# Kernel tuning notes

Measured on AMD Instinct MI355X. Metric: run time of the kernel, lower is better.

The kernel has to match this reference:

```python
import jax, jax.numpy as jnp
import numpy as np

N, F, K, E = 50000, 128, 8, 1600000


def setup_inputs() -> dict:
    key = jax.random.key(0)
    k1, k2, k3, k4 = jax.random.split(key, 4)
    x = jax.random.normal(k1, (N, F), dtype=jnp.float32)
    adj = jax.random.randint(k2, (2, E), 0, N, dtype=jnp.int64)
    e = jax.random.normal(k3, (N, K), dtype=jnp.float32)
    stdv = 1.0 / np.sqrt(F)  # reset_parameters: uniform(-stdv, stdv)
    weights = jax.random.uniform(k4, (K, 2 * F, F), dtype=jnp.float32,
                                 minval=-stdv, maxval=stdv)
    return {"x": x, "adj": adj, "e": e, "weights": weights}


def _gcn_conv(x, row, col, n_nodes):
    # degree of each node as a message *destination* (col) -- matches torch degree(col, N)
    deg = jax.ops.segment_sum(jnp.ones(row.shape[0], x.dtype), col,
                              num_segments=n_nodes)
    val = (1.0 / jnp.sqrt(deg[col])) * (1.0 / jnp.sqrt(deg[row]))
    val = jnp.nan_to_num(val, nan=0.0, posinf=0.0, neginf=0.0)
    # SparseTensor(row=col, col=row) @ x : aggregate x[row] into col
    msg = val[:, None] * x[row]           # [E, F] gather
    return jax.ops.segment_sum(msg, col, num_segments=n_nodes)  # [N, F] scatter


def reference(x, adj, e, weights):
    n_nodes = x.shape[0]
    row, col = adj[0], adj[1]
    hi = _gcn_conv(x, row, col, n_nodes)                  # [N, F]
    hi = jnp.concatenate([hi, x], axis=1)                 # [N, 2F]
    # torch: repeat hi K times, bmm with [K,2F,F], transpose -> [N, K, F]
    outputs = jnp.einsum('nf,kfo->nko', hi, weights)      # [N, K, F]
    out = jnp.sum(e[:, :, None] * outputs, axis=1)        # gating sum over K
    out = out + x                                         # residual
    return out
```

## Files before the change

### kernel.cpp

```cpp
#include <hip/hip_runtime.h>
#include <hip/hip_bf16.h>

typedef __bf16 bf16_t;
typedef __bf16 bf16x8 __attribute__((ext_vector_type(8)));
typedef float f32x4 __attribute__((ext_vector_type(4)));
typedef float f32x2 __attribute__((ext_vector_type(2)));

#define F 128
#define KEXP 8
#define BM 256
#define BSTG 32768

#define NB 196
#define CAP 12288
#define CH 8192

__global__ __launch_bounds__(256) void k_binA(const int* __restrict__ row,
    const int* __restrict__ col, int* __restrict__ cursor,
    int* __restrict__ region, int E){
  __shared__ int stage[CH];
  __shared__ unsigned char stageb[CH];
  __shared__ int hist4[4][NB];
  __shared__ int lcur4[4][NB];
  int tid = threadIdx.x, wid = tid >> 6;
  int base = blockIdx.x * CH;
  int cnt = min(CH, E - base);
  for (int i = tid; i < 4*NB; i += 256) ((int*)hist4)[i] = 0;
  __syncthreads();
  for (int i = tid; i < cnt; i += 256){
    int r = row[base+i], c = col[base+i];
    stage[i] = (r << 8) | (c & 255);
    stageb[i] = (unsigned char)(c >> 8);
    atomicAdd(&hist4[wid][c >> 8], 1);
  }
  __syncthreads();
  for (int b = tid; b < NB; b += 256){
    int h0 = hist4[0][b], h1 = hist4[1][b], h2 = hist4[2][b], h3 = hist4[3][b];
    int gbase = atomicAdd(&cursor[b], h0+h1+h2+h3) + b*CAP;
    lcur4[0][b] = gbase;
    lcur4[1][b] = gbase + h0;
    lcur4[2][b] = gbase + h0 + h1;
    lcur4[3][b] = gbase + h0 + h1 + h2;
  }
  __syncthreads();
  for (int i = tid; i < cnt; i += 256){
    int b = stageb[i];
    int pos = atomicAdd(&lcur4[wid][b], 1);
    region[pos] = stage[i];
  }
}

__global__ void k_bstart(const int* __restrict__ cursor, int* __restrict__ bstart,
                         int* __restrict__ offs, int Nn){
  __shared__ int lds[256];
  int t = threadIdx.x;
  int c = (t < NB) ? cursor[t] : 0;
  lds[t] = c; __syncthreads();
  for (int off=1; off<256; off<<=1){
    int u = (t>=off) ? lds[t-off] : 0;
    __syncthreads();
    lds[t] += u;
    __syncthreads();
  }
  if (t < NB) bstart[t] = lds[t] - c;
  if (t == NB-1){ bstart[NB] = lds[t]; offs[Nn] = lds[t]; }
}

__global__ __launch_bounds__(256) void k_binB(const int* __restrict__ region,
    const int* __restrict__ cursor, const int* __restrict__ bstart,
    int* __restrict__ deg, int* __restrict__ offs, int* __restrict__ bucket,
    int Nn){
  __shared__ int hist4[4][256];
  __shared__ int loff[256];
  __shared__ int lcur4[4][256];
  int b = blockIdx.x, t = threadIdx.x, wid = t >> 6;
  int cnt = cursor[b];
  const int* src = region + b*CAP;
  for (int i = t; i < 4*256; i += 256) ((int*)hist4)[i] = 0;
  __syncthreads();
  for (int i = t; i < cnt; i += 256) atomicAdd(&hist4[wid][src[i] & 255], 1);
  __syncthreads();
  int h0 = hist4[0][t], h1 = hist4[1][t], h2 = hist4[2][t], h3 = hist4[3][t];
  int v = h0 + h1 + h2 + h3;
  loff[t] = v;
  __syncthreads();
  for (int off=1; off<256; off<<=1){
    int u = (t>=off) ? loff[t-off] : 0;
    __syncthreads();
    loff[t] += u;
    __syncthreads();
  }
  int excl = loff[t] - v;
  int gb = bstart[b];
  int node = b*256 + t;
  if (node < Nn){ deg[node] = v; offs[node] = gb + excl; }
  lcur4[0][t] = gb + excl;
  lcur4[1][t] = gb + excl + h0;
  lcur4[2][t] = gb + excl + h0 + h1;
  lcur4[3][t] = gb + excl + h0 + h1 + h2;
  __syncthreads();
  for (int i = t; i < cnt; i += 256){
    int p = src[i];
    int pos = atomicAdd(&lcur4[wid][p & 255], 1);
    bucket[pos] = p >> 8;
  }
}

__global__ void k_prep(const float* __restrict__ x, const int* __restrict__ deg,
                       unsigned int* __restrict__ xs8, const float* __restrict__ W,
                       bf16_t* __restrict__ Wt, int Nn, int xsB){
  int tid = threadIdx.x;
  if ((int)blockIdx.x < xsB){
    int i = blockIdx.x*256 + tid;
    if (i < Nn*16){
      int n = i >> 4;
      int d = deg[n];
      float dr = d>0 ? rsqrtf((float)d) : 0.f;
      const float4 f0 = *reinterpret_cast<const float4*>(&x[(size_t)i*8]);
      const float4 f1 = *reinterpret_cast<const float4*>(&x[(size_t)i*8+4]);
      unsigned int lo, hi2;
      lo  = __builtin_amdgcn_cvt_pk_fp8_f32(dr*f0.x, dr*f0.y, 0,  false);
      lo  = __builtin_amdgcn_cvt_pk_fp8_f32(dr*f0.z, dr*f0.w, lo, true);
      hi2 = __builtin_amdgcn_cvt_pk_fp8_f32(dr*f1.x, dr*f1.y, 0,  false);
      hi2 = __builtin_amdgcn_cvt_pk_fp8_f32(dr*f1.z, dr*f1.w, hi2, true);
      xs8[(size_t)i*2]     = lo;
      xs8[(size_t)i*2 + 1] = hi2;
    }
  } else {
    int i8 = (blockIdx.x - xsB)*256 + tid;
    if (i8 < 32768){
      int kk   = i8 >> 12;
      int frag = (i8 >> 6) & 63;
      int lane = i8 & 63;
      int ks = frag >> 3, cg = frag & 7;
      int n  = cg*16 + (lane & 15);
      int f0 = ks*32 + (lane >> 4)*8;
      bf16x8 v;
      #pragma unroll
      for (int j=0;j<8;j++)
        v[j] = (bf16_t)W[(size_t)kk*32768 + (size_t)(f0+j)*128 + n];
      *reinterpret_cast<bf16x8*>(&Wt[(size_t)i8*8]) = v;
    }
  }
}

__global__ __launch_bounds__(256) void k_agg(const unsigned int* __restrict__ xs8,
    const int* __restrict__ offs, const int* __restrict__ bucket,
    bf16_t* __restrict__ hi, int Nn){
  int wid = threadIdx.x >> 6, lane = threadIdx.x & 63;
  int g = lane >> 4, j16 = lane & 15;
  int n = blockIdx.x*16 + wid*4 + g;
  if (n >= Nn) return;
  int o0 = offs[n], o1 = offs[n+1];
  float acc[8] = {0.f,0.f,0.f,0.f,0.f,0.f,0.f,0.f};
  int nr = (o1 - o0 + 7) >> 3;
  int j = o0;
  for (int r = 0; r < nr; r++, j += 8){
    int idx[8];
    #pragma unroll
    for (int t=0;t<8;t++) idx[t] = bucket[min(j+t, o1-1)];
    uint2 v[8];
    #pragma unroll
    for (int t=0;t<8;t++)
      v[t] = *reinterpret_cast<const uint2*>(
          reinterpret_cast<const unsigned char*>(xs8) + (size_t)idx[t]*F + j16*8);
    #pragma unroll
    for (int t=0;t<8;t++){
      float m = (j+t < o1) ? 1.f : 0.f;
      f32x2 p0 = __builtin_amdgcn_cvt_pk_f32_fp8(v[t].x, false);
      f32x2 p1 = __builtin_amdgcn_cvt_pk_f32_fp8(v[t].x, true);
      f32x2 p2 = __builtin_amdgcn_cvt_pk_f32_fp8(v[t].y, false);
      f32x2 p3 = __builtin_amdgcn_cvt_pk_f32_fp8(v[t].y, true);
      acc[0] += m*p0.x; acc[1] += m*p0.y;
      acc[2] += m*p1.x; acc[3] += m*p1.y;
      acc[4] += m*p2.x; acc[5] += m*p2.y;
      acc[6] += m*p3.x; acc[7] += m*p3.y;
    }
  }
  int dn = o1 - o0;
  float dc = dn>0 ? rsqrtf((float)dn) : 0.f;
  bf16x8 o;
  #pragma unroll
  for (int i=0;i<8;i++) o[i] = (bf16_t)(dc*acc[i]);
  *reinterpret_cast<bf16x8*>(&hi[(size_t)n*F + j16*8]) = o;
}

#define MFMA_BF16 __builtin_amdgcn_mfma_f32_16x16x32_bf16

__global__ __launch_bounds__(512, 2) void k_gemm(
    const bf16_t* __restrict__ hi, const float* __restrict__ x,
    const float* __restrict__ e, const bf16_t* __restrict__ Wt,
    float* __restrict__ out, int Nn)
{
  extern __shared__ __align__(16) char smem[];
  bf16_t* b_s  = (bf16_t*)smem;
  float*  e_sT = (float*)(smem + 2*BSTG*2);
  const int tid = threadIdx.x;
  const int base = blockIdx.x * BM;
  const int lane = tid & 63, wid = tid >> 6;
  const int r16 = lane & 15, kc = lane >> 4;

  {
    const bf16_t* src = Wt;
    bf16_t* dst = b_s;
    #pragma unroll
    for (int i=0;i<8;i++){
      int u = tid + i*512;
      __builtin_amdgcn_global_load_lds(
          (const __attribute__((address_space(1))) void*)(src + (size_t)u*8),
          (__attribute__((address_space(3))) void*)(dst + (size_t)u*8),
          16, 0, 0);
    }
  }

  for (int i = tid; i < KEXP*BM; i += 512){
    int kk = i >> 8, row = i & (BM-1);
    int srow = min(base + row, Nn-1);
    e_sT[kk*BM + row] = e[(size_t)srow*KEXP + kk];
  }

  int rA = min(base + wid*32 + r16,      Nn-1);
  int rB = min(base + wid*32 + 16 + r16, Nn-1);
  bf16x8 a[2][8];
  #pragma unroll
  for (int ks=0; ks<4; ks++){
    a[0][ks] = *reinterpret_cast<const bf16x8*>(&hi[(size_t)rA*F + ks*32 + kc*8]);
    a[1][ks] = *reinterpret_cast<const bf16x8*>(&hi[(size_t)rB*F + ks*32 + kc*8]);
  }
  #pragma unroll
  for (int ks=0; ks<4; ks++){
    const float4 f0 = *reinterpret_cast<const float4*>(&x[(size_t)rA*F + ks*32 + kc*8]);
    const float4 f1 = *reinterpret_cast<const float4*>(&x[(size_t)rA*F + ks*32 + kc*8 + 4]);
    bf16x8 v;
    v[0]=(bf16_t)f0.x; v[1]=(bf16_t)f0.y; v[2]=(bf16_t)f0.z; v[3]=(bf16_t)f0.w;
    v[4]=(bf16_t)f1.x; v[5]=(bf16_t)f1.y; v[6]=(bf16_t)f1.z; v[7]=(bf16_t)f1.w;
    a[0][4+ks] = v;
    const float4 g0 = *reinterpret_cast<const float4*>(&x[(size_t)rB*F + ks*32 + kc*8]);
    const float4 g1 = *reinterpret_cast<const float4*>(&x[(size_t)rB*F + ks*32 + kc*8 + 4]);
    bf16x8 u;
    u[0]=(bf16_t)g0.x; u[1]=(bf16_t)g0.y; u[2]=(bf16_t)g0.z; u[3]=(bf16_t)g0.w;
    u[4]=(bf16_t)g1.x; u[5]=(bf16_t)g1.y; u[6]=(bf16_t)g1.z; u[7]=(bf16_t)g1.w;
    a[1][4+ks] = u;
  }

  f32x4 acc[2][8];
  #pragma unroll
  for (int rg=0;rg<2;rg++)
    #pragma unroll
    for (int cg=0;cg<8;cg++) acc[rg][cg] = (f32x4){0.f,0.f,0.f,0.f};
  const f32x4 fz = (f32x4){0.f,0.f,0.f,0.f};

  asm volatile("s_waitcnt vmcnt(0) lgkmcnt(0)" ::: "memory");
  __builtin_amdgcn_s_barrier();

  for (int kk=0; kk<8; kk++){
    if (kk < 7){
      const bf16_t* src = Wt + (size_t)(kk+1)*BSTG;
      bf16_t* dst = b_s + ((kk+1)&1)*BSTG;
      #pragma unroll
      for (int i=0;i<8;i++){
        int u = tid + i*512;
        __builtin_amdgcn_global_load_lds(
            (const __attribute__((address_space(1))) void*)(src + (size_t)u*8),
            (__attribute__((address_space(3))) void*)(dst + (size_t)u*8),
            16, 0, 0);
      }
      asm volatile("s_waitcnt vmcnt(8)" ::: "memory");
    } else {
      asm volatile("s_waitcnt vmcnt(0)" ::: "memory");
    }
    __builtin_amdgcn_s_barrier();

    const bf16_t* buf = b_s + (kk&1)*BSTG;
    f32x4 ev0 = *reinterpret_cast<const f32x4*>(&e_sT[kk*BM + wid*32 + kc*4]);
    f32x4 ev1 = *reinterpret_cast<const f32x4*>(&e_sT[kk*BM + wid*32 + 16 + kc*4]);

    #pragma unroll
    for (int cgh=0; cgh<2; cgh++){
      f32x4 ck[2][4];
      __builtin_amdgcn_s_setprio(1);
      #pragma unroll
      for (int cg=0; cg<4; cg++){
        bf16x8 b = *reinterpret_cast<const bf16x8*>(
            &buf[(size_t)(cgh*4 + cg)*512 + lane*8]);
        ck[0][cg] = MFMA_BF16(a[0][0], b, fz, 0, 0, 0);
        ck[1][cg] = MFMA_BF16(a[1][0], b, fz, 0, 0, 0);
      }
      #pragma unroll
      for (int ks=1; ks<8; ks++)
        #pragma unroll
        for (int cg=0; cg<4; cg++){
          bf16x8 b = *reinterpret_cast<const bf16x8*>(
              &buf[(size_t)(ks*8 + cgh*4 + cg)*512 + lane*8]);
          ck[0][cg] = MFMA_BF16(a[0][ks], b, ck[0][cg], 0, 0, 0);
          ck[1][cg] = MFMA_BF16(a[1][ks], b, ck[1][cg], 0, 0, 0);
        }
      __builtin_amdgcn_s_setprio(0);
      #pragma unroll
      for (int cg=0; cg<4; cg++)
        #pragma unroll
        for (int r=0; r<4; r++){
          acc[0][cgh*4+cg][r] += ev0[r]*ck[0][cg][r];
          acc[1][cgh*4+cg][r] += ev1[r]*ck[1][cg][r];
        }
    }

    __builtin_amdgcn_s_barrier();
  }

  #pragma unroll
  for (int rg=0; rg<2; rg++){
    #pragma unroll
    for (int cg=0; cg<8; cg++){
      int ocol = cg*16 + r16;
      #pragma unroll
      for (int r=0; r<4; r++){
        int node = base + wid*32 + rg*16 + kc*4 + r;
        if (node < Nn)
          out[(size_t)node*F + ocol] = acc[rg][cg][r] + x[(size_t)node*F + ocol];
      }
    }
  }
}

extern "C" void kernel_launch(void* const* d_in, const int* in_sizes, int n_in,
                              void* d_out, int out_size, void* d_ws, size_t ws_size,
                              hipStream_t stream){
  const float* x  = (const float*)d_in[0];
  const int*  adj = (const int*)d_in[1];
  const float* e  = (const float*)d_in[2];
  const float* W  = (const float*)d_in[3];
  float* out = (float*)d_out;
  int Nn = in_sizes[0] / F;
  int E  = in_sizes[1] / 2;
  const int* rowp = adj;
  const int* colp = adj + E;

  char* w = (char*)d_ws;
  auto alloc = [&](size_t b){ char* p = w; w += (b + 255) & ~(size_t)255; return p; };
  int* deg     = (int*)alloc((size_t)Nn*4);
  int* offs    = (int*)alloc(((size_t)Nn+1)*4);
  int* cursor  = (int*)alloc((size_t)NB*4);
  int* bstart  = (int*)alloc((size_t)(NB+1)*4);
  int* bucket  = (int*)alloc((size_t)E*4);
  char* uni    = alloc((size_t)NB*CAP*4);
  int* region  = (int*)uni;
  unsigned int* xs8 = (unsigned int*)uni;
  bf16_t* hi   = (bf16_t*)alloc((size_t)Nn*F*2);
  bf16_t* Wt   = (bf16_t*)alloc((size_t)2048*F*2);

  const int smem_bytes = 2*BSTG*2 + KEXP*BM*4;
  hipFuncSetAttribute((const void*)k_gemm,
                      hipFuncAttributeMaxDynamicSharedMemorySize, smem_bytes);

  int nchunks = (E + CH - 1) / CH;
  int xsB = (Nn*16 + 255)/256;
  hipMemsetAsync(cursor, 0, (size_t)NB*4, stream);
  k_binA<<<nchunks, 256, 0, stream>>>(rowp, colp, cursor, region, E);
  k_bstart<<<1, 256, 0, stream>>>(cursor, bstart, offs, Nn);
  k_binB<<<NB, 256, 0, stream>>>(region, cursor, bstart, deg, offs, bucket, Nn);
  k_prep<<<xsB + 128, 256, 0, stream>>>(x, deg, xs8, W, Wt, Nn, xsB);
  k_agg<<<(Nn+15)/16, 256, 0, stream>>>(xs8, offs, bucket, hi, Nn);
  k_gemm<<<(Nn+BM-1)/BM, 512, smem_bytes, stream>>>(hi, x, e, Wt, out, Nn);
}
```

Before: 135.5 us.

## Retile gather-GEMM into 4x2 warp grid with half-size weight stages

The gating GEMM now splits the block's 8 waves into a 4x2 grid: each wave covers 64 rows and 64 output columns instead of 32 rows and all 128 columns. Each B fragment read from LDS now feeds four MFMAs instead of two, which roughly halves shared-memory read traffic. The weight pipeline becomes 16 stages of 16K elements, the hi half and then the x half per expert, and the prep kernel rewrites the weight layout to match. This cuts LDS per block from about 136KB to about 72KB, so two blocks can share a CU. The costs are twice as many barriers, and the x operand is now loaded and converted partway through the loop, which can stall.

```diff
diff --git a/kernel.cpp b/kernel.cpp
--- a/kernel.cpp
+++ b/kernel.cpp
@@ -9,7 +9,7 @@
 #define F 128
 #define KEXP 8
 #define BM 256
-#define BSTG 32768
+#define SSTG 16384
 
 #define NB 196
 #define CAP 12288
@@ -129,12 +129,14 @@
   } else {
     int i8 = (blockIdx.x - xsB)*256 + tid;
     if (i8 < 32768){
-      int kk   = i8 >> 12;
-      int frag = (i8 >> 6) & 63;
-      int lane = i8 & 63;
-      int ks = frag >> 3, cg = frag & 7;
-      int n  = cg*16 + (lane & 15);
-      int f0 = ks*32 + (lane >> 4)*8;
+      int st   = i8 >> 11;
+      int g    = i8 & 2047;
+      int frag = g >> 6;
+      int lane = g & 63;
+      int h = st >> 3, kk = st & 7;
+      int ksl = frag >> 3, cgg = frag & 7;
+      int n  = cgg*16 + (lane & 15);
+      int f0 = h*128 + ksl*32 + (lane >> 4)*8;
       bf16x8 v;
       #pragma unroll
       for (int j=0;j<8;j++)
@@ -194,23 +196,20 @@
 {
   extern __shared__ __align__(16) char smem[];
   bf16_t* b_s  = (bf16_t*)smem;
-  float*  e_sT = (float*)(smem + 2*BSTG*2);
+  float*  e_sT = (float*)(smem + 2*SSTG*2);
   const int tid = threadIdx.x;
   const int base = blockIdx.x * BM;
   const int lane = tid & 63, wid = tid >> 6;
+  const int rw = wid >> 1, cw = wid & 1;
   const int r16 = lane & 15, kc = lane >> 4;
 
-  {
-    const bf16_t* src = Wt;
-    bf16_t* dst = b_s;
-    #pragma unroll
-    for (int i=0;i<8;i++){
-      int u = tid + i*512;
-      __builtin_amdgcn_global_load_lds(
-          (const __attribute__((address_space(1))) void*)(src + (size_t)u*8),
-          (__attribute__((address_space(3))) void*)(dst + (size_t)u*8),
-          16, 0, 0);
-    }
+  #pragma unroll
+  for (int i=0;i<4;i++){
+    int u = tid + i*512;
+    __builtin_amdgcn_global_load_lds(
+        (const __attribute__((address_space(1))) void*)(Wt + (size_t)u*8),
+        (__attribute__((address_space(3))) void*)(b_s + (size_t)u*8),
+        16, 0, 0);
   }
 
   for (int i = tid; i < KEXP*BM; i += 512){
@@ -219,103 +218,106 @@
     e_sT[kk*BM + row] = e[(size_t)srow*KEXP + kk];
   }
 
-  int rA = min(base + wid*32 + r16,      Nn-1);
-  int rB = min(base + wid*32 + 16 + r16, Nn-1);
-  bf16x8 a[2][8];
-  #pragma unroll
-  for (int ks=0; ks<4; ks++){
-    a[0][ks] = *reinterpret_cast<const bf16x8*>(&hi[(size_t)rA*F + ks*32 + kc*8]);
-    a[1][ks] = *reinterpret_cast<const bf16x8*>(&hi[(size_t)rB*F + ks*32 + kc*8]);
-  }
-  #pragma unroll
-  for (int ks=0; ks<4; ks++){
-    const float4 f0 = *reinterpret_cast<const float4*>(&x[(size_t)rA*F + ks*32 + kc*8]);
-    const float4 f1 = *reinterpret_cast<const float4*>(&x[(size_t)rA*F + ks*32 + kc*8 + 4]);
-    bf16x8 v;
-    v[0]=(bf16_t)f0.x; v[1]=(bf16_t)f0.y; v[2]=(bf16_t)f0.z; v[3]=(bf16_t)f0.w;
-    v[4]=(bf16_t)f1.x; v[5]=(bf16_t)f1.y; v[6]=(bf16_t)f1.z; v[7]=(bf16_t)f1.w;
-    a[0][4+ks] = v;
-    const float4 g0 = *reinterpret_cast<const float4*>(&x[(size_t)rB*F + ks*32 + kc*8]);
-    const float4 g1 = *reinterpret_cast<const float4*>(&x[(size_t)rB*F + ks*32 + kc*8 + 4]);
-    bf16x8 u;
-    u[0]=(bf16_t)g0.x; u[1]=(bf16_t)g0.y; u[2]=(bf16_t)g0.z; u[3]=(bf16_t)g0.w;
-    u[4]=(bf16_t)g1.x; u[5]=(bf16_t)g1.y; u[6]=(bf16_t)g1.z; u[7]=(bf16_t)g1.w;
-    a[1][4+ks] = u;
-  }
-
-  f32x4 acc[2][8];
-  #pragma unroll
-  for (int rg=0;rg<2;rg++)
-    #pragma unroll
-    for (int cg=0;cg<8;cg++) acc[rg][cg] = (f32x4){0.f,0.f,0.f,0.f};
+  int rr[4];
+  #pragma unroll
+  for (int rg=0; rg<4; rg++) rr[rg] = min(base + rw*64 + rg*16 + r16, Nn-1);
+  bf16x8 a[4][4];
+  #pragma unroll
+  for (int rg=0; rg<4; rg++)
+    #pragma unroll
+    for (int ks=0; ks<4; ks++)
+      a[rg][ks] = *reinterpret_cast<const bf16x8*>(
+          &hi[(size_t)rr[rg]*F + ks*32 + kc*8]);
+
+  f32x4 acc[4][4];
+  #pragma unroll
+  for (int rg=0;rg<4;rg++)
+    #pragma unroll
+    for (int cg=0;cg<4;cg++) acc[rg][cg] = (f32x4){0.f,0.f,0.f,0.f};
   const f32x4 fz = (f32x4){0.f,0.f,0.f,0.f};
 
   asm volatile("s_waitcnt vmcnt(0) lgkmcnt(0)" ::: "memory");
   __builtin_amdgcn_s_barrier();
 
-  for (int kk=0; kk<8; kk++){
-    if (kk < 7){
-      const bf16_t* src = Wt + (size_t)(kk+1)*BSTG;
-      bf16_t* dst = b_s + ((kk+1)&1)*BSTG;
-      #pragma unroll
-      for (int i=0;i<8;i++){
+  for (int st=0; st<16; st++){
+    if (st == 8){
+      #pragma unroll
+      for (int rg=0; rg<4; rg++)
+        #pragma unroll
+        for (int ks=0; ks<4; ks++){
+          const float4 f0 = *reinterpret_cast<const float4*>(
+              &x[(size_t)rr[rg]*F + ks*32 + kc*8]);
+          const float4 f1 = *reinterpret_cast<const float4*>(
+              &x[(size_t)rr[rg]*F + ks*32 + kc*8 + 4]);
+          bf16x8 v;
+          v[0]=(bf16_t)f0.x; v[1]=(bf16_t)f0.y; v[2]=(bf16_t)f0.z; v[3]=(bf16_t)f0.w;
+          v[4]=(bf16_t)f1.x; v[5]=(bf16_t)f1.y; v[6]=(bf16_t)f1.z; v[7]=(bf16_t)f1.w;
+          a[rg][ks] = v;
+        }
+    }
+    if (st < 15){
+      const bf16_t* src = Wt + (size_t)(st+1)*SSTG;
+      bf16_t* dst = b_s + ((st+1)&1)*SSTG;
+      #pragma unroll
+      for (int i=0;i<4;i++){
         int u = tid + i*512;
         __builtin_amdgcn_global_load_lds(
             (const __attribute__((address_space(1))) void*)(src + (size_t)u*8),
             (__attribute__((address_space(3))) void*)(dst + (size_t)u*8),
             16, 0, 0);
       }
-      asm volatile("s_waitcnt vmcnt(8)" ::: "memory");
+      asm volatile("s_waitcnt vmcnt(4)" ::: "memory");
     } else {
       asm volatile("s_waitcnt vmcnt(0)" ::: "memory");
     }
     __builtin_amdgcn_s_barrier();
 
-    const bf16_t* buf = b_s + (kk&1)*BSTG;
-    f32x4 ev0 = *reinterpret_cast<const f32x4*>(&e_sT[kk*BM + wid*32 + kc*4]);
-    f32x4 ev1 = *reinterpret_cast<const f32x4*>(&e_sT[kk*BM + wid*32 + 16 + kc*4]);
-
-    #pragma unroll
-    for (int cgh=0; cgh<2; cgh++){
-      f32x4 ck[2][4];
-      __builtin_amdgcn_s_setprio(1);
+    const bf16_t* buf = b_s + (st&1)*SSTG;
+    f32x4 ck[4][4];
+    __builtin_amdgcn_s_setprio(1);
+    #pragma unroll
+    for (int cg=0; cg<4; cg++){
+      bf16x8 b = *reinterpret_cast<const bf16x8*>(
+          &buf[(size_t)(cw*4 + cg)*512 + lane*8]);
+      #pragma unroll
+      for (int rg=0; rg<4; rg++)
+        ck[rg][cg] = MFMA_BF16(a[rg][0], b, fz, 0, 0, 0);
+    }
+    #pragma unroll
+    for (int ks=1; ks<4; ks++)
       #pragma unroll
       for (int cg=0; cg<4; cg++){
         bf16x8 b = *reinterpret_cast<const bf16x8*>(
-            &buf[(size_t)(cgh*4 + cg)*512 + lane*8]);
-        ck[0][cg] = MFMA_BF16(a[0][0], b, fz, 0, 0, 0);
-        ck[1][cg] = MFMA_BF16(a[1][0], b, fz, 0, 0, 0);
+            &buf[(size_t)(ks*8 + cw*4 + cg)*512 + lane*8]);
+        #pragma unroll
+        for (int rg=0; rg<4; rg++)
+          ck[rg][cg] = MFMA_BF16(a[rg][ks], b, ck[rg][cg], 0, 0, 0);
       }
-      #pragma unroll
-      for (int ks=1; ks<8; ks++)
-        #pragma unroll
-        for (int cg=0; cg<4; cg++){
-          bf16x8 b = *reinterpret_cast<const bf16x8*>(
-              &buf[(size_t)(ks*8 + cgh*4 + cg)*512 + lane*8]);
-          ck[0][cg] = MFMA_BF16(a[0][ks], b, ck[0][cg], 0, 0, 0);
-          ck[1][cg] = MFMA_BF16(a[1][ks], b, ck[1][cg], 0, 0, 0);
-        }
-      __builtin_amdgcn_s_setprio(0);
+    __builtin_amdgcn_s_setprio(0);
+
+    const int kk = st & 7;
+    #pragma unroll
+    for (int rg=0; rg<4; rg++){
+      f32x4 ev = *reinterpret_cast<const f32x4*>(
+          &e_sT[kk*BM + rw*64 + rg*16 + kc*4]);
       #pragma unroll
       for (int cg=0; cg<4; cg++)
         #pragma unroll
-        for (int r=0; r<4; r++){
-          acc[0][cgh*4+cg][r] += ev0[r]*ck[0][cg][r];
-          acc[1][cgh*4+cg][r] += ev1[r]*ck[1][cg][r];
-        }
+        for (int r=0; r<4; r++)
+          acc[rg][cg][r] += ev[r]*ck[rg][cg][r];
     }
 
     __builtin_amdgcn_s_barrier();
   }
 
   #pragma unroll
-  for (int rg=0; rg<2; rg++){
-    #pragma unroll
-    for (int cg=0; cg<8; cg++){
-      int ocol = cg*16 + r16;
+  for (int rg=0; rg<4; rg++){
+    #pragma unroll
+    for (int cg=0; cg<4; cg++){
+      int ocol = cw*64 + cg*16 + r16;
       #pragma unroll
       for (int r=0; r<4; r++){
-        int node = base + wid*32 + rg*16 + kc*4 + r;
+        int node = base + rw*64 + rg*16 + kc*4 + r;
         if (node < Nn)
           out[(size_t)node*F + ocol] = acc[rg][cg][r] + x[(size_t)node*F + ocol];
       }
@@ -349,7 +351,7 @@
   bf16_t* hi   = (bf16_t*)alloc((size_t)Nn*F*2);
   bf16_t* Wt   = (bf16_t*)alloc((size_t)2048*F*2);
 
-  const int smem_bytes = 2*BSTG*2 + KEXP*BM*4;
+  const int smem_bytes = 2*SSTG*2 + KEXP*BM*4;
   hipFuncSetAttribute((const void*)k_gemm,
                       hipFuncAttributeMaxDynamicSharedMemorySize, smem_bytes);
 
```

After: 143.6 us. 1.06x slower.

## Drop bucket prefix-scan kernel, use fixed-capacity bucket offsets, fuse weight prep into binning

Applied to the files above, without the earlier changes.

Removes the single-block k_bstart prefix-scan kernel by giving each coarse bin a fixed CAP-sized region in the bucket array, so offsets become b*CAP+excl and k_agg reads deg instead of offs[n+1]. The weight transpose/convert moves into extra blocks of k_binA, and the binning chunk size is halved to launch more blocks. The setprio hints in the GEMM are removed. This saves a launch and a serialization point at the cost of a larger, sparser bucket array.

```diff
diff --git a/kernel.cpp b/kernel.cpp
--- a/kernel.cpp
+++ b/kernel.cpp
@@ -13,11 +13,29 @@
 
 #define NB 196
 #define CAP 12288
-#define CH 8192
+#define CH 4096
 
 __global__ __launch_bounds__(256) void k_binA(const int* __restrict__ row,
     const int* __restrict__ col, int* __restrict__ cursor,
-    int* __restrict__ region, int E){
+    int* __restrict__ region, const float* __restrict__ W,
+    bf16_t* __restrict__ Wt, int E, int nbin){
+  if ((int)blockIdx.x >= nbin){
+    int i8 = (blockIdx.x - nbin)*256 + threadIdx.x;
+    if (i8 < 32768){
+      int kk   = i8 >> 12;
+      int frag = (i8 >> 6) & 63;
+      int lane = i8 & 63;
+      int ks = frag >> 3, cg = frag & 7;
+      int n  = cg*16 + (lane & 15);
+      int f0 = ks*32 + (lane >> 4)*8;
+      bf16x8 v;
+      #pragma unroll
+      for (int j=0;j<8;j++)
+        v[j] = (bf16_t)W[(size_t)kk*32768 + (size_t)(f0+j)*128 + n];
+      *reinterpret_cast<bf16x8*>(&Wt[(size_t)i8*8]) = v;
+    }
+    return;
+  }
   __shared__ int stage[CH];
   __shared__ unsigned char stageb[CH];
   __shared__ int hist4[4][NB];
@@ -50,26 +68,9 @@
   }
 }
 
-__global__ void k_bstart(const int* __restrict__ cursor, int* __restrict__ bstart,
-                         int* __restrict__ offs, int Nn){
-  __shared__ int lds[256];
-  int t = threadIdx.x;
-  int c = (t < NB) ? cursor[t] : 0;
-  lds[t] = c; __syncthreads();
-  for (int off=1; off<256; off<<=1){
-    int u = (t>=off) ? lds[t-off] : 0;
-    __syncthreads();
-    lds[t] += u;
-    __syncthreads();
-  }
-  if (t < NB) bstart[t] = lds[t] - c;
-  if (t == NB-1){ bstart[NB] = lds[t]; offs[Nn] = lds[t]; }
-}
-
 __global__ __launch_bounds__(256) void k_binB(const int* __restrict__ region,
-    const int* __restrict__ cursor, const int* __restrict__ bstart,
-    int* __restrict__ deg, int* __restrict__ offs, int* __restrict__ bucket,
-    int Nn){
+    const int* __restrict__ cursor, int* __restrict__ deg,
+    int* __restrict__ offs, int* __restrict__ bucket, int Nn){
   __shared__ int hist4[4][256];
   __shared__ int loff[256];
   __shared__ int lcur4[4][256];
@@ -91,7 +92,7 @@
     __syncthreads();
   }
   int excl = loff[t] - v;
-  int gb = bstart[b];
+  int gb = b*CAP;
   int node = b*256 + t;
   if (node < Nn){ deg[node] = v; offs[node] = gb + excl; }
   lcur4[0][t] = gb + excl;
@@ -106,54 +107,37 @@
   }
 }
 
-__global__ void k_prep(const float* __restrict__ x, const int* __restrict__ deg,
-                       unsigned int* __restrict__ xs8, const float* __restrict__ W,
-                       bf16_t* __restrict__ Wt, int Nn, int xsB){
-  int tid = threadIdx.x;
-  if ((int)blockIdx.x < xsB){
-    int i = blockIdx.x*256 + tid;
-    if (i < Nn*16){
-      int n = i >> 4;
-      int d = deg[n];
-      float dr = d>0 ? rsqrtf((float)d) : 0.f;
-      const float4 f0 = *reinterpret_cast<const float4*>(&x[(size_t)i*8]);
-      const float4 f1 = *reinterpret_cast<const float4*>(&x[(size_t)i*8+4]);
-      unsigned int lo, hi2;
-      lo  = __builtin_amdgcn_cvt_pk_fp8_f32(dr*f0.x, dr*f0.y, 0,  false);
-      lo  = __builtin_amdgcn_cvt_pk_fp8_f32(dr*f0.z, dr*f0.w, lo, true);
-      hi2 = __builtin_amdgcn_cvt_pk_fp8_f32(dr*f1.x, dr*f1.y, 0,  false);
-      hi2 = __builtin_amdgcn_cvt_pk_fp8_f32(dr*f1.z, dr*f1.w, hi2, true);
-      xs8[(size_t)i*2]     = lo;
-      xs8[(size_t)i*2 + 1] = hi2;
-    }
-  } else {
-    int i8 = (blockIdx.x - xsB)*256 + tid;
-    if (i8 < 32768){
-      int kk   = i8 >> 12;
-      int frag = (i8 >> 6) & 63;
-      int lane = i8 & 63;
-      int ks = frag >> 3, cg = frag & 7;
-      int n  = cg*16 + (lane & 15);
-      int f0 = ks*32 + (lane >> 4)*8;
-      bf16x8 v;
-      #pragma unroll
-      for (int j=0;j<8;j++)
-        v[j] = (bf16_t)W[(size_t)kk*32768 + (size_t)(f0+j)*128 + n];
-      *reinterpret_cast<bf16x8*>(&Wt[(size_t)i8*8]) = v;
-    }
+__global__ void k_prep_xs(const float* __restrict__ x, const int* __restrict__ deg,
+                          unsigned int* __restrict__ xs8, int Nn){
+  int i = blockIdx.x*256 + threadIdx.x;
+  if (i < Nn*16){
+    int n = i >> 4;
+    int d = deg[n];
+    float dr = d>0 ? rsqrtf((float)d) : 0.f;
+    const float4 f0 = *reinterpret_cast<const float4*>(&x[(size_t)i*8]);
+    const float4 f1 = *reinterpret_cast<const float4*>(&x[(size_t)i*8+4]);
+    unsigned int lo, hi2;
+    lo  = __builtin_amdgcn_cvt_pk_fp8_f32(dr*f0.x, dr*f0.y, 0,  false);
+    lo  = __builtin_amdgcn_cvt_pk_fp8_f32(dr*f0.z, dr*f0.w, lo, true);
+    hi2 = __builtin_amdgcn_cvt_pk_fp8_f32(dr*f1.x, dr*f1.y, 0,  false);
+    hi2 = __builtin_amdgcn_cvt_pk_fp8_f32(dr*f1.z, dr*f1.w, hi2, true);
+    xs8[(size_t)i*2]     = lo;
+    xs8[(size_t)i*2 + 1] = hi2;
   }
 }
 
 __global__ __launch_bounds__(256) void k_agg(const unsigned int* __restrict__ xs8,
-    const int* __restrict__ offs, const int* __restrict__ bucket,
-    bf16_t* __restrict__ hi, int Nn){
+    const int* __restrict__ offs, const int* __restrict__ deg,
+    const int* __restrict__ bucket, bf16_t* __restrict__ hi, int Nn){
   int wid = threadIdx.x >> 6, lane = threadIdx.x & 63;
   int g = lane >> 4, j16 = lane & 15;
   int n = blockIdx.x*16 + wid*4 + g;
   if (n >= Nn) return;
-  int o0 = offs[n], o1 = offs[n+1];
+  int o0 = offs[n];
+  int dn = deg[n];
+  int o1 = o0 + dn;
   float acc[8] = {0.f,0.f,0.f,0.f,0.f,0.f,0.f,0.f};
-  int nr = (o1 - o0 + 7) >> 3;
+  int nr = (dn + 7) >> 3;
   int j = o0;
   for (int r = 0; r < nr; r++, j += 8){
     int idx[8];
@@ -177,7 +161,6 @@
       acc[6] += m*p3.x; acc[7] += m*p3.y;
     }
   }
-  int dn = o1 - o0;
   float dc = dn>0 ? rsqrtf((float)dn) : 0.f;
   bf16x8 o;
   #pragma unroll
@@ -200,17 +183,13 @@
   const int lane = tid & 63, wid = tid >> 6;
   const int r16 = lane & 15, kc = lane >> 4;
 
-  {
-    const bf16_t* src = Wt;
-    bf16_t* dst = b_s;
-    #pragma unroll
-    for (int i=0;i<8;i++){
-      int u = tid + i*512;
-      __builtin_amdgcn_global_load_lds(
-          (const __attribute__((address_space(1))) void*)(src + (size_t)u*8),
-          (__attribute__((address_space(3))) void*)(dst + (size_t)u*8),
-          16, 0, 0);
-    }
+  #pragma unroll
+  for (int i=0;i<8;i++){
+    int u = tid + i*512;
+    __builtin_amdgcn_global_load_lds(
+        (const __attribute__((address_space(1))) void*)(Wt + (size_t)u*8),
+        (__attribute__((address_space(3))) void*)(b_s + (size_t)u*8),
+        16, 0, 0);
   }
 
   for (int i = tid; i < KEXP*BM; i += 512){
@@ -278,7 +257,6 @@
     #pragma unroll
     for (int cgh=0; cgh<2; cgh++){
       f32x4 ck[2][4];
-      __builtin_amdgcn_s_setprio(1);
       #pragma unroll
       for (int cg=0; cg<4; cg++){
         bf16x8 b = *reinterpret_cast<const bf16x8*>(
@@ -295,7 +273,6 @@
           ck[0][cg] = MFMA_BF16(a[0][ks], b, ck[0][cg], 0, 0, 0);
           ck[1][cg] = MFMA_BF16(a[1][ks], b, ck[1][cg], 0, 0, 0);
         }
-      __builtin_amdgcn_s_setprio(0);
       #pragma unroll
       for (int cg=0; cg<4; cg++)
         #pragma unroll
@@ -339,10 +316,9 @@
   char* w = (char*)d_ws;
   auto alloc = [&](size_t b){ char* p = w; w += (b + 255) & ~(size_t)255; return p; };
   int* deg     = (int*)alloc((size_t)Nn*4);
-  int* offs    = (int*)alloc(((size_t)Nn+1)*4);
+  int* offs    = (int*)alloc((size_t)Nn*4);
   int* cursor  = (int*)alloc((size_t)NB*4);
-  int* bstart  = (int*)alloc((size_t)(NB+1)*4);
-  int* bucket  = (int*)alloc((size_t)E*4);
+  int* bucket  = (int*)alloc((size_t)NB*CAP*4);
   char* uni    = alloc((size_t)NB*CAP*4);
   int* region  = (int*)uni;
   unsigned int* xs8 = (unsigned int*)uni;
@@ -353,13 +329,12 @@
   hipFuncSetAttribute((const void*)k_gemm,
                       hipFuncAttributeMaxDynamicSharedMemorySize, smem_bytes);
 
-  int nchunks = (E + CH - 1) / CH;
-  int xsB = (Nn*16 + 255)/256;
+  int nbin = (E + CH - 1) / CH;
+  int xsB  = (Nn*16 + 255)/256;
   hipMemsetAsync(cursor, 0, (size_t)NB*4, stream);
-  k_binA<<<nchunks, 256, 0, stream>>>(rowp, colp, cursor, region, E);
-  k_bstart<<<1, 256, 0, stream>>>(cursor, bstart, offs, Nn);
-  k_binB<<<NB, 256, 0, stream>>>(region, cursor, bstart, deg, offs, bucket, Nn);
-  k_prep<<<xsB + 128, 256, 0, stream>>>(x, deg, xs8, W, Wt, Nn, xsB);
-  k_agg<<<(Nn+15)/16, 256, 0, stream>>>(xs8, offs, bucket, hi, Nn);
+  k_binA<<<nbin + 128, 256, 0, stream>>>(rowp, colp, cursor, region, W, Wt, E, nbin);
+  k_binB<<<NB, 256, 0, stream>>>(region, cursor, deg, offs, bucket, Nn);
+  k_prep_xs<<<xsB, 256, 0, stream>>>(x, deg, xs8, Nn);
+  k_agg<<<(Nn+15)/16, 256, 0, stream>>>(xs8, offs, deg, bucket, hi, Nn);
   k_gemm<<<(Nn+BM-1)/BM, 512, smem_bytes, stream>>>(hi, x, e, Wt, out, Nn);
 }
```

Result: faster. 132.3 us (median of 3 runs) (-2.4%).
